# Performance work log

Hardware: AMD Instinct MI355X
Metric: run time of the kernel (lower is better)

The kernel has to match this reference:

```python
import jax, jax.numpy as jnp
import numpy as np

NEG_SLOPE = 0.2
EPS = 1e-16

N_NODES = 50000
N_EDGES = 1600000
IN_CH = 256
HID = 16
HEADS = 2


def setup_inputs() -> dict:
    key = jax.random.key(0)
    ks = jax.random.split(key, 12)
    s = lambda k, shape, scale=0.1: jax.random.normal(k, shape, dtype=jnp.float32) * scale
    x = jax.random.normal(ks[0], (N_NODES, IN_CH), dtype=jnp.float32)
    edge_index = jax.random.randint(ks[1], (2, N_EDGES), 0, N_NODES, dtype=jnp.int64)
    return {
        "x": x,
        "edge_index": edge_index,
        "W1": s(ks[2], (IN_CH, HEADS * HID)),
        "att_src1": s(ks[3], (HEADS, HID)),
        "att_dst1": s(ks[4], (HEADS, HID)),
        "b1": jnp.zeros((HEADS * HID,), jnp.float32),
        "W2": s(ks[5], (HEADS * HID, HID)),
        "att_src2": s(ks[6], (1, HID)),
        "att_dst2": s(ks[7], (1, HID)),
        "b2": jnp.zeros((HID,), jnp.float32),
        "Wm1": s(ks[8], (2 * HID, HID)),
        "bm1": jnp.zeros((HID,), jnp.float32),
        "Wm2": s(ks[9], (HID, 1)),
        "bm2": jnp.zeros((1,), jnp.float32),
    }


def gat_conv(x, src, dst, W, att_src, att_dst, bias, heads, out_ch, concat):
    # x: [N, F] -> h: [N, H, C]
    n = x.shape[0]
    h = (x @ W).reshape(n, heads, out_ch)
    # per-node attention logits [N, H]
    a_src = jnp.sum(h * att_src, axis=-1)
    a_dst = jnp.sum(h * att_dst, axis=-1)
    # per-edge logits: message j (src) -> i (dst); softmax grouped by dst
    e = a_src[src] + a_dst[dst]                      # [E, H]
    e = jax.nn.leaky_relu(e, NEG_SLOPE)
    e_max = jax.ops.segment_max(e, dst, num_segments=n)
    e_exp = jnp.exp(e - e_max[dst])
    denom = jax.ops.segment_sum(e_exp, dst, num_segments=n)
    alpha = e_exp / (denom[dst] + EPS)               # [E, H]
    msg = alpha[:, :, None] * h[src]                 # [E, H, C]
    out = jax.ops.segment_sum(msg, dst, num_segments=n)  # [N, H, C]
    out = out.reshape(n, heads * out_ch) if concat else out.mean(axis=1)
    return out + bias


def reference(x, edge_index, W1, att_src1, att_dst1, b1,
              W2, att_src2, att_dst2, b2, Wm1, bm1, Wm2, bm2):
    src, dst = edge_index[0], edge_index[1]
    # eval mode: feature/attention dropout are identity
    h = gat_conv(x, src, dst, W1, att_src1, att_dst1, b1, HEADS, HID, concat=True)
    h = jax.nn.elu(h)
    h = gat_conv(h, src, dst, W2, att_src2, att_dst2, b2, 1, HID, concat=False)
    # edge MLP on gathered (src, dst) node pairs
    ef = jnp.concatenate([h[src], h[dst]], axis=-1)  # [E, 2*HID]
    ef = jax.nn.relu(ef @ Wm1 + bm1)
    flow = (ef @ Wm2 + bm2).squeeze(-1)              # [E]
    return jax.nn.relu(flow)
```

## Files before the change

kernel.cpp:

```cpp
#include <hip/hip_runtime.h>
#include <hip/hip_bf16.h>
#include <hip/hip_fp16.h>

#define N_NODES 50000
#define N_EDGES 1600000
#define IN_CH 256
#define NEG_SLOPE 0.2f
#define EPS_F 1e-16f
#define CNT_PAD 16
#define CAP 128
#define NBK 196
#define CAPB 10240
#define PCHUNK 3125
#define KTILE 64
#define XS_PITCH (KTILE + 4)

__device__ __forceinline__ float lrelu(float x) {
    return x > 0.f ? x : NEG_SLOPE * x;
}

__device__ __forceinline__ float2 h2f(unsigned int w) {
    __half2 h;
    *reinterpret_cast<unsigned int*>(&h) = w;
    return __half22float2(h);
}

__device__ __forceinline__ unsigned int f2h2(float a, float b) {
    __half2 h = __floats2half2_rn(a, b);
    return *reinterpret_cast<unsigned int*>(&h);
}

__device__ __forceinline__ int detect_i64(const int* __restrict__ ei) {
    const int lane = threadIdx.x & 63;
    const unsigned long long b = __ballot(ei[2 * lane + 1] != 0);
    return b == 0ull ? 1 : 0;
}

__device__ __forceinline__ int ld_src(const int* ei, int f, int e) {
    return f ? ei[2 * (size_t)e] : ei[e];
}
__device__ __forceinline__ int ld_dst(const int* ei, int f, int e) {
    return f ? ei[2 * (size_t)N_EDGES + 2 * (size_t)e]
             : ei[(size_t)N_EDGES + e];
}

__global__ __launch_bounds__(1024) void k_part(const int* __restrict__ ei,
                                               int* __restrict__ gcnt,
                                               int2* __restrict__ bseg)
{
    __shared__ int hist[NBK];
    __shared__ int cur[NBK];
    const int t = threadIdx.x;
    const int f = detect_i64(ei);
    for (int j = t; j < NBK; j += 1024) hist[j] = 0;
    __syncthreads();
    const int e0 = blockIdx.x * PCHUNK;
    const int e1 = min(e0 + PCHUNK, N_EDGES);
    for (int e = e0 + t; e < e1; e += 1024)
        atomicAdd(&hist[ld_dst(ei, f, e) >> 8], 1);
    __syncthreads();
    for (int j = t; j < NBK; j += 1024)
        cur[j] = j * CAPB + atomicAdd(&gcnt[j], hist[j]);
    __syncthreads();
    for (int e = e0 + t; e < e1; e += 1024) {
        const int s = ld_src(ei, f, e);
        const int d = ld_dst(ei, f, e);
        const int bk = d >> 8;
        const int pos = atomicAdd(&cur[bk], 1);
        if (pos - bk * CAPB < CAPB) bseg[pos] = make_int2(s, d);
    }
}

__global__ __launch_bounds__(1024) void k_sub(const int* __restrict__ gcnt,
                                              const int2* __restrict__ bseg,
                                              int* __restrict__ cnt,
                                              int* __restrict__ csr_src)
{
    __shared__ int cur[256];
    const int b = blockIdx.x;
    const int t = threadIdx.x;
    if (t < 256) cur[t] = 0;
    __syncthreads();
    const int count = min(gcnt[b], CAPB);
    const int2* seg = bseg + (size_t)b * CAPB;
    for (int i = t; i < count; i += 1024) {
        const int2 e = seg[i];
        const int slot = atomicAdd(&cur[e.y & 255], 1);
        if (slot < CAP) csr_src[((size_t)e.y << 7) + slot] = e.x;
    }
    __syncthreads();
    if (t < 256) {
        const int n = b * 256 + t;
        if (n < N_NODES) cnt[(size_t)n * CNT_PAD] = min(cur[t], CAP);
    }
}

__global__ __launch_bounds__(256) void k1_gemm1(
    const float* __restrict__ x, const float* __restrict__ W1,
    const float* __restrict__ att_src1, const float* __restrict__ att_dst1,
    __half* __restrict__ h1, float* __restrict__ a_src1, float* __restrict__ a_dst1)
{
    __shared__ float w1s[IN_CH * 32];
    __shared__ float xs[64 * XS_PITCH];
    __shared__ float attss[32], attds[32];
    const int t = threadIdx.x;
    for (int i = t; i < IN_CH * 32; i += 256) w1s[i] = W1[i];
    if (t < 32) { attss[t] = att_src1[t]; attds[t] = att_dst1[t]; }
    const int row0 = blockIdx.x * 64;
    const int colq = t & 7, c4 = colq * 4;
    const int rp = t >> 3;
    const int r0 = rp * 2, r1 = r0 + 1;
    float4 a0 = make_float4(0.f, 0.f, 0.f, 0.f);
    float4 a1 = make_float4(0.f, 0.f, 0.f, 0.f);
    for (int kb = 0; kb < IN_CH; kb += KTILE) {
        __syncthreads();
        #pragma unroll
        for (int i = 0; i < 4; ++i) {
            const int idx = t + 256 * i;
            const int r = idx >> 4, p = idx & 15;
            const int row = row0 + r;
            float4 vv = make_float4(0.f, 0.f, 0.f, 0.f);
            if (row < N_NODES)
                vv = *(const float4*)(x + (size_t)row * IN_CH + kb + p * 4);
            *(float4*)(&xs[r * XS_PITCH + p * 4]) = vv;
        }
        __syncthreads();
        #pragma unroll 8
        for (int kt = 0; kt < KTILE; ++kt) {
            const float xv0 = xs[r0 * XS_PITCH + kt];
            const float xv1 = xs[r1 * XS_PITCH + kt];
            const float4 wv = *(const float4*)(&w1s[(kb + kt) * 32 + c4]);
            a0.x += xv0 * wv.x; a0.y += xv0 * wv.y;
            a0.z += xv0 * wv.z; a0.w += xv0 * wv.w;
            a1.x += xv1 * wv.x; a1.y += xv1 * wv.y;
            a1.z += xv1 * wv.z; a1.w += xv1 * wv.w;
        }
    }
    const int row_a = row0 + r0, row_b = row0 + r1;
    if (row_a < N_NODES) {
        uint2 p; p.x = f2h2(a0.x, a0.y); p.y = f2h2(a0.z, a0.w);
        *(uint2*)(h1 + (size_t)row_a * 32 + c4) = p;
    }
    if (row_b < N_NODES) {
        uint2 p; p.x = f2h2(a1.x, a1.y); p.y = f2h2(a1.z, a1.w);
        *(uint2*)(h1 + (size_t)row_b * 32 + c4) = p;
    }
    float sa0 = a0.x * attss[c4] + a0.y * attss[c4 + 1]
              + a0.z * attss[c4 + 2] + a0.w * attss[c4 + 3];
    float sd0 = a0.x * attds[c4] + a0.y * attds[c4 + 1]
              + a0.z * attds[c4 + 2] + a0.w * attds[c4 + 3];
    float sa1 = a1.x * attss[c4] + a1.y * attss[c4 + 1]
              + a1.z * attss[c4 + 2] + a1.w * attss[c4 + 3];
    float sd1 = a1.x * attds[c4] + a1.y * attds[c4 + 1]
              + a1.z * attds[c4 + 2] + a1.w * attds[c4 + 3];
    sa0 += __shfl_xor(sa0, 1); sa0 += __shfl_xor(sa0, 2);
    sd0 += __shfl_xor(sd0, 1); sd0 += __shfl_xor(sd0, 2);
    sa1 += __shfl_xor(sa1, 1); sa1 += __shfl_xor(sa1, 2);
    sd1 += __shfl_xor(sd1, 1); sd1 += __shfl_xor(sd1, 2);
    const int head = colq >> 2;
    if ((colq & 3) == 0) {
        if (row_a < N_NODES) {
            a_src1[row_a * 2 + head] = sa0;
            a_dst1[row_a * 2 + head] = sd0;
        }
        if (row_b < N_NODES) {
            a_src1[row_b * 2 + head] = sa1;
            a_dst1[row_b * 2 + head] = sd1;
        }
    }
}

__global__ __launch_bounds__(256) void k_agg1f(
    const int* __restrict__ cnt, const int* __restrict__ csr_src,
    const float* __restrict__ a_src1, const float* __restrict__ a_dst1,
    const __half* __restrict__ h1,
    const float* __restrict__ b1, const float* __restrict__ W2,
    const float* __restrict__ att_src2, const float* __restrict__ att_dst2,
    __half* __restrict__ h2, float* __restrict__ a_src2, float* __restrict__ a_dst2)
{
    __shared__ float w2s[32 * 16];
    __shared__ float b1s[32], as2[16], ad2[16];
    __shared__ float act_s[4][32];
    const int t = threadIdx.x;
    for (int i = t; i < 512; i += 256) w2s[i] = W2[i];
    if (t < 32) b1s[t] = b1[t];
    if (t < 16) { as2[t] = att_src2[t]; ad2[t] = att_dst2[t]; }

    const int wid = (blockIdx.x * 256 + t) >> 6;
    const int lane = t & 63;
    const int wv = t >> 6;
    const int active = (wid < N_NODES);
    const int len = active ? min(cnt[(size_t)wid * CNT_PAD], CAP) : 0;
    const int beg = wid << 7, end = beg + len;
    float2 ad = make_float2(0.f, 0.f);
    if (active) ad = *(const float2*)(a_dst1 + 2 * (size_t)wid);
    const int slot = lane >> 4, chp = lane & 15;
    const int head = chp >> 3;
    const float adh = head ? ad.y : ad.x;
    const int rep = ((chp & 7) == 0);
    const unsigned int* __restrict__ h1u = (const unsigned int*)h1;
    float accx = 0.f, accy = 0.f, sw = 0.f;
    int i = beg + slot;
    for (; i + 28 < end; i += 32) {
        int s[8]; float a[8]; unsigned int hw[8]; float w[8];
        #pragma unroll
        for (int j = 0; j < 8; ++j) s[j] = csr_src[i + 4 * j];
        #pragma unroll
        for (int j = 0; j < 8; ++j) a[j] = a_src1[2 * (size_t)s[j] + head];
        #pragma unroll
        for (int j = 0; j < 8; ++j) hw[j] = h1u[(size_t)s[j] * 16 + chp];
        #pragma unroll
        for (int j = 0; j < 8; ++j) w[j] = __expf(lrelu(a[j] + adh));
        float wsum = 0.f;
        #pragma unroll
        for (int j = 0; j < 8; ++j) {
            const float2 hf = h2f(hw[j]);
            wsum += w[j];
            accx += w[j] * hf.x; accy += w[j] * hf.y;
        }
        if (rep) sw += wsum;
    }
    for (; i + 12 < end; i += 16) {
        int s[4]; float a[4]; unsigned int hw[4]; float w[4];
        #pragma unroll
        for (int j = 0; j < 4; ++j) s[j] = csr_src[i + 4 * j];
        #pragma unroll
        for (int j = 0; j < 4; ++j) a[j] = a_src1[2 * (size_t)s[j] + head];
        #pragma unroll
        for (int j = 0; j < 4; ++j) hw[j] = h1u[(size_t)s[j] * 16 + chp];
        #pragma unroll
        for (int j = 0; j < 4; ++j) w[j] = __expf(lrelu(a[j] + adh));
        float wsum = 0.f;
        #pragma unroll
        for (int j = 0; j < 4; ++j) {
            const float2 hf = h2f(hw[j]);
            wsum += w[j];
            accx += w[j] * hf.x; accy += w[j] * hf.y;
        }
        if (rep) sw += wsum;
    }
    for (; i < end; i += 4) {
        const int s = csr_src[i];
        const float w = __expf(lrelu(a_src1[2 * (size_t)s + head] + adh));
        if (rep) sw += w;
        const float2 hf = h2f(h1u[(size_t)s * 16 + chp]);
        accx += w * hf.x; accy += w * hf.y;
    }
    sw += __shfl_xor(sw, 16); sw += __shfl_xor(sw, 32);
    const float swh = __shfl(sw, head << 3);
    accx += __shfl_xor(accx, 16); accx += __shfl_xor(accx, 32);
    accy += __shfl_xor(accy, 16); accy += __shfl_xor(accy, 32);
    const float inv = 1.f / (swh + EPS_F);
    if (lane < 16) {
        float ax = accx * inv + b1s[2 * chp];
        float ay = accy * inv + b1s[2 * chp + 1];
        ax = ax > 0.f ? ax : expm1f(ax);
        ay = ay > 0.f ? ay : expm1f(ay);
        act_s[wv][2 * chp] = ax;
        act_s[wv][2 * chp + 1] = ay;
    }
    __syncthreads();
    const int j = lane & 15;
    float acc2 = 0.f;
    #pragma unroll
    for (int k = 0; k < 32; ++k) acc2 += act_s[wv][k] * w2s[k * 16 + j];
    if (lane < 16 && active) h2[(size_t)wid * 16 + j] = __float2half(acc2);
    float sa = acc2 * as2[j], sd = acc2 * ad2[j];
    sa += __shfl_xor(sa, 1); sa += __shfl_xor(sa, 2);
    sa += __shfl_xor(sa, 4); sa += __shfl_xor(sa, 8);
    sd += __shfl_xor(sd, 1); sd += __shfl_xor(sd, 2);
    sd += __shfl_xor(sd, 4); sd += __shfl_xor(sd, 8);
    if (lane == 0 && active) { a_src2[wid] = sa; a_dst2[wid] = sd; }
}

__global__ __launch_bounds__(256) void k_agg2f(
    const int* __restrict__ cnt, const int* __restrict__ csr_src,
    const float* __restrict__ a_src2, const float* __restrict__ a_dst2,
    const __half* __restrict__ h2,
    const float* __restrict__ b2, const float* __restrict__ Wm1,
    const float* __restrict__ bm1,
    __half* __restrict__ u, __half* __restrict__ v)
{
    __shared__ float wa[16 * 16], wb[16 * 16];
    __shared__ float b2s[16], bm1s[16];
    __shared__ float act_s[4][16];
    const int t = threadIdx.x;
    if (t < 256) { wa[t] = Wm1[t]; wb[t] = Wm1[256 + t]; }
    if (t < 16) { b2s[t] = b2[t]; bm1s[t] = bm1[t]; }

    const int wid = (blockIdx.x * 256 + t) >> 6;
    const int lane = t & 63;
    const int wv = t >> 6;
    const int active = (wid < N_NODES);
    const int len = active ? min(cnt[(size_t)wid * CNT_PAD], CAP) : 0;
    const int beg = wid << 7, end = beg + len;
    const float ad = active ? a_dst2[wid] : 0.f;
    const int slot = lane >> 3, chp = lane & 7;
    const int rep = (chp == 0);
    const unsigned int* __restrict__ h2u = (const unsigned int*)h2;
    float accx = 0.f, accy = 0.f, sw = 0.f;
    int i = beg + slot;
    for (; i + 24 < end; i += 32) {
        int s[4]; float a[4]; unsigned int hw[4]; float w[4];
        #pragma unroll
        for (int j = 0; j < 4; ++j) s[j] = csr_src[i + 8 * j];
        #pragma unroll
        for (int j = 0; j < 4; ++j) a[j] = a_src2[s[j]];
        #pragma unroll
        for (int j = 0; j < 4; ++j) hw[j] = h2u[(size_t)s[j] * 8 + chp];
        #pragma unroll
        for (int j = 0; j < 4; ++j) w[j] = __expf(lrelu(a[j] + ad));
        float wsum = 0.f;
        #pragma unroll
        for (int j = 0; j < 4; ++j) {
            const float2 hf = h2f(hw[j]);
            wsum += w[j];
            accx += w[j] * hf.x; accy += w[j] * hf.y;
        }
        if (rep) sw += wsum;
    }
    for (; i < end; i += 8) {
        const int s = csr_src[i];
        const float w = __expf(lrelu(a_src2[s] + ad));
        if (rep) sw += w;
        const float2 hf = h2f(h2u[(size_t)s * 8 + chp]);
        accx += w * hf.x; accy += w * hf.y;
    }
    sw += __shfl_xor(sw, 8); sw += __shfl_xor(sw, 16); sw += __shfl_xor(sw, 32);
    const float swt = __shfl(sw, 0);
    accx += __shfl_xor(accx, 8); accx += __shfl_xor(accx, 16); accx += __shfl_xor(accx, 32);
    accy += __shfl_xor(accy, 8); accy += __shfl_xor(accy, 16); accy += __shfl_xor(accy, 32);
    const float inv = 1.f / (swt + EPS_F);
    if (lane < 8) {
        float2 o;
        o.x = accx * inv + b2s[2 * chp];
        o.y = accy * inv + b2s[2 * chp + 1];
        *(float2*)(&act_s[wv][2 * chp]) = o;
    }
    __syncthreads();
    const int c = lane & 15;
    float su = bm1s[c], sv = 0.f;
    #pragma unroll
    for (int k = 0; k < 16; ++k) {
        const float a = act_s[wv][k];
        su += a * wa[k * 16 + c];
        sv += a * wb[k * 16 + c];
    }
    if (lane < 16 && active) {
        u[(size_t)wid * 16 + c] = __float2half(su);
        v[(size_t)wid * 16 + c] = __float2half(sv);
    }
}

__global__ __launch_bounds__(256) void k7_lite(
    const int* __restrict__ ei,
    const __half* __restrict__ u, const __half* __restrict__ v,
    const float* __restrict__ Wm2, const float* __restrict__ bm2,
    float* __restrict__ out)
{
    __shared__ float wm2s[16];
    __shared__ float bm2s;
    const int t = threadIdx.x;
    const int f = detect_i64(ei);
    if (t < 16) wm2s[t] = Wm2[t];
    if (t == 0) bm2s = bm2[0];
    __syncthreads();
    const int e = blockIdx.x * 256 + t;
    if (e >= N_EDGES) return;
    const int s = ld_src(ei, f, e);
    const int d = ld_dst(ei, f, e);
    const uint4* up = (const uint4*)(u + (size_t)s * 16);
    const uint4* vp = (const uint4*)(v + (size_t)d * 16);
    const uint4 ua = up[0], ub = up[1];
    const uint4 va = vp[0], vb = vp[1];
    float fl = bm2s;
    unsigned int uw[8] = {ua.x, ua.y, ua.z, ua.w, ub.x, ub.y, ub.z, ub.w};
    unsigned int vw[8] = {va.x, va.y, va.z, va.w, vb.x, vb.y, vb.z, vb.w};
    #pragma unroll
    for (int i = 0; i < 8; ++i) {
        const float2 a = h2f(uw[i]);
        const float2 b = h2f(vw[i]);
        fl += fmaxf(a.x + b.x, 0.f) * wm2s[2 * i];
        fl += fmaxf(a.y + b.y, 0.f) * wm2s[2 * i + 1];
    }
    out[e] = fmaxf(fl, 0.f);
}

extern "C" void kernel_launch(void* const* d_in, const int* in_sizes, int n_in,
                              void* d_out, int out_size, void* d_ws, size_t ws_size,
                              hipStream_t stream)
{
    const float* x        = (const float*)d_in[0];
    const int*   ei       = (const int*)d_in[1];
    const float* W1       = (const float*)d_in[2];
    const float* att_src1 = (const float*)d_in[3];
    const float* att_dst1 = (const float*)d_in[4];
    const float* b1       = (const float*)d_in[5];
    const float* W2       = (const float*)d_in[6];
    const float* att_src2 = (const float*)d_in[7];
    const float* att_dst2 = (const float*)d_in[8];
    const float* b2       = (const float*)d_in[9];
    const float* Wm1      = (const float*)d_in[10];
    const float* bm1      = (const float*)d_in[11];
    const float* Wm2      = (const float*)d_in[12];
    const float* bm2      = (const float*)d_in[13];

    float* ws = (float*)d_ws;
    size_t off = 0;
    __half* h1 = (__half*)(ws + off); off += 16 * (size_t)N_NODES;
    float* a_src1 = ws + off; off += 2  * (size_t)N_NODES;
    float* a_dst1 = ws + off; off += 2  * (size_t)N_NODES;
    float* out1_dead = ws + off; off += 32 * (size_t)N_NODES;
    __half* h2 = (__half*)(ws + off); off += 16 * (size_t)N_NODES;
    float* a_src2 = ws + off; off += 1  * (size_t)N_NODES;
    float* a_dst2 = ws + off; off += 1  * (size_t)N_NODES;
    float* out2_dead = ws + off; off += 16 * (size_t)N_NODES;
    __half* u = (__half*)(ws + off); off += 8 * (size_t)N_NODES;
    __half* v = (__half*)(ws + off); off += 8 * (size_t)N_NODES;
    int* cnt     = (int*)(ws + off); off += (size_t)N_NODES * CNT_PAD;
    int* csr_src = (int*)(ws + off); off += (size_t)N_NODES * CAP;
    int* gcnt    = (int*)(ws + off); off += 256;
    int* flag    = (int*)(ws + off); off += 64;
    (void)out1_dead; (void)out2_dead; (void)flag;
    int2* bseg = (int2*)ws;

    hipMemsetAsync(gcnt, 0, 256 * sizeof(int), stream);
    k_part<<<(N_EDGES + PCHUNK - 1) / PCHUNK, 1024, 0, stream>>>(ei, gcnt, bseg);
    k_sub<<<NBK, 1024, 0, stream>>>(gcnt, bseg, cnt, csr_src);

    k1_gemm1<<<(N_NODES + 63) / 64, 256, 0, stream>>>(
        x, W1, att_src1, att_dst1, h1, a_src1, a_dst1);
    k_agg1f<<<(N_NODES + 3) / 4, 256, 0, stream>>>(
        cnt, csr_src, a_src1, a_dst1, h1, b1, W2, att_src2, att_dst2,
        h2, a_src2, a_dst2);
    k_agg2f<<<(N_NODES + 3) / 4, 256, 0, stream>>>(
        cnt, csr_src, a_src2, a_dst2, h2, b2, Wm1, bm1, u, v);
    k7_lite<<<(N_EDGES + 255) / 256, 256, 0, stream>>>(
        ei, u, v, Wm2, bm2, (float*)d_out);
}
```

Measured before the change: 259.3 us.

## Map one node per 16-lane group in layer-1 aggregation and cache edges in registers

The layer-1 aggregation kernel now gives each 16-lane group its own destination node, four nodes per wave and 16 per block, instead of one node per 64-lane wave. This removes the cross-slot shuffle reductions and the underused lanes on short adjacency lists, but lanes in a wave now diverge on list length and idle lanes are masked. The partition kernel loads each thread's edges once into registers and reuses them for both the histogram and scatter passes, removing a second global read of edge_index. The bucketed edge scratch also gets its own workspace region instead of aliasing the start of the workspace, and the dead buffers are dropped.

Result: faster. 251.6 us (-3.0%).

```diff
diff --git a/kernel.cpp b/kernel.cpp
--- a/kernel.cpp
+++ b/kernel.cpp
@@ -56,18 +56,26 @@
     __syncthreads();
     const int e0 = blockIdx.x * PCHUNK;
     const int e1 = min(e0 + PCHUNK, N_EDGES);
-    for (int e = e0 + t; e < e1; e += 1024)
-        atomicAdd(&hist[ld_dst(ei, f, e) >> 8], 1);
+    int es[4], ed[4];
+    int ne = 0;
+    #pragma unroll
+    for (int q = 0; q < 4; ++q) {
+        const int e = e0 + t + 1024 * q;
+        if (e < e1) {
+            es[ne] = ld_src(ei, f, e);
+            ed[ne] = ld_dst(ei, f, e);
+            ++ne;
+        }
+    }
+    for (int q = 0; q < ne; ++q) atomicAdd(&hist[ed[q] >> 8], 1);
     __syncthreads();
     for (int j = t; j < NBK; j += 1024)
         cur[j] = j * CAPB + atomicAdd(&gcnt[j], hist[j]);
     __syncthreads();
-    for (int e = e0 + t; e < e1; e += 1024) {
-        const int s = ld_src(ei, f, e);
-        const int d = ld_dst(ei, f, e);
-        const int bk = d >> 8;
+    for (int q = 0; q < ne; ++q) {
+        const int bk = ed[q] >> 8;
         const int pos = atomicAdd(&cur[bk], 1);
-        if (pos - bk * CAPB < CAPB) bseg[pos] = make_int2(s, d);
+        if (pos - bk * CAPB < CAPB) bseg[pos] = make_int2(es[q], ed[q]);
     }
 }
 
@@ -180,97 +188,69 @@
 {
     __shared__ float w2s[32 * 16];
     __shared__ float b1s[32], as2[16], ad2[16];
-    __shared__ float act_s[4][32];
+    __shared__ float act_s[16][33];
     const int t = threadIdx.x;
     for (int i = t; i < 512; i += 256) w2s[i] = W2[i];
     if (t < 32) b1s[t] = b1[t];
     if (t < 16) { as2[t] = att_src2[t]; ad2[t] = att_dst2[t]; }
 
-    const int wid = (blockIdx.x * 256 + t) >> 6;
     const int lane = t & 63;
     const int wv = t >> 6;
-    const int active = (wid < N_NODES);
-    const int len = active ? min(cnt[(size_t)wid * CNT_PAD], CAP) : 0;
-    const int beg = wid << 7, end = beg + len;
-    float2 ad = make_float2(0.f, 0.f);
-    if (active) ad = *(const float2*)(a_dst1 + 2 * (size_t)wid);
-    const int slot = lane >> 4, chp = lane & 15;
+    const int g = lane >> 4;
+    const int chp = lane & 15;
     const int head = chp >> 3;
-    const float adh = head ? ad.y : ad.x;
-    const int rep = ((chp & 7) == 0);
+    const int node = blockIdx.x * 16 + wv * 4 + g;
+    const int active = (node < N_NODES);
+    const int len = active ? min(cnt[(size_t)node * CNT_PAD], CAP) : 0;
+    const int beg = node << 7;
+    const float adh = active ? a_dst1[2 * (size_t)node + head] : 0.f;
     const unsigned int* __restrict__ h1u = (const unsigned int*)h1;
     float accx = 0.f, accy = 0.f, sw = 0.f;
-    int i = beg + slot;
-    for (; i + 28 < end; i += 32) {
+    for (int bi = 0; __any(bi < len); bi += 8) {
         int s[8]; float a[8]; unsigned int hw[8]; float w[8];
         #pragma unroll
-        for (int j = 0; j < 8; ++j) s[j] = csr_src[i + 4 * j];
+        for (int j = 0; j < 8; ++j) {
+            int sv = csr_src[beg + bi + j];
+            s[j] = (bi + j < len) ? sv : 0;
+        }
         #pragma unroll
         for (int j = 0; j < 8; ++j) a[j] = a_src1[2 * (size_t)s[j] + head];
         #pragma unroll
         for (int j = 0; j < 8; ++j) hw[j] = h1u[(size_t)s[j] * 16 + chp];
         #pragma unroll
-        for (int j = 0; j < 8; ++j) w[j] = __expf(lrelu(a[j] + adh));
-        float wsum = 0.f;
+        for (int j = 0; j < 8; ++j)
+            w[j] = (bi + j < len) ? __expf(lrelu(a[j] + adh)) : 0.f;
         #pragma unroll
         for (int j = 0; j < 8; ++j) {
             const float2 hf = h2f(hw[j]);
-            wsum += w[j];
+            sw += w[j];
             accx += w[j] * hf.x; accy += w[j] * hf.y;
         }
-        if (rep) sw += wsum;
-    }
-    for (; i + 12 < end; i += 16) {
-        int s[4]; float a[4]; unsigned int hw[4]; float w[4];
-        #pragma unroll
-        for (int j = 0; j < 4; ++j) s[j] = csr_src[i + 4 * j];
-        #pragma unroll
-        for (int j = 0; j < 4; ++j) a[j] = a_src1[2 * (size_t)s[j] + head];
-        #pragma unroll
-        for (int j = 0; j < 4; ++j) hw[j] = h1u[(size_t)s[j] * 16 + chp];
-        #pragma unroll
-        for (int j = 0; j < 4; ++j) w[j] = __expf(lrelu(a[j] + adh));
-        float wsum = 0.f;
-        #pragma unroll
-        for (int j = 0; j < 4; ++j) {
-            const float2 hf = h2f(hw[j]);
-            wsum += w[j];
-            accx += w[j] * hf.x; accy += w[j] * hf.y;
-        }
-        if (rep) sw += wsum;
-    }
-    for (; i < end; i += 4) {
-        const int s = csr_src[i];
-        const float w = __expf(lrelu(a_src1[2 * (size_t)s + head] + adh));
-        if (rep) sw += w;
-        const float2 hf = h2f(h1u[(size_t)s * 16 + chp]);
-        accx += w * hf.x; accy += w * hf.y;
-    }
-    sw += __shfl_xor(sw, 16); sw += __shfl_xor(sw, 32);
-    const float swh = __shfl(sw, head << 3);
-    accx += __shfl_xor(accx, 16); accx += __shfl_xor(accx, 32);
-    accy += __shfl_xor(accy, 16); accy += __shfl_xor(accy, 32);
-    const float inv = 1.f / (swh + EPS_F);
-    if (lane < 16) {
+    }
+    const float inv = 1.f / (sw + EPS_F);
+    const int nl = wv * 4 + g;
+    {
         float ax = accx * inv + b1s[2 * chp];
         float ay = accy * inv + b1s[2 * chp + 1];
         ax = ax > 0.f ? ax : expm1f(ax);
         ay = ay > 0.f ? ay : expm1f(ay);
-        act_s[wv][2 * chp] = ax;
-        act_s[wv][2 * chp + 1] = ay;
-    }
-    __syncthreads();
-    const int j = lane & 15;
+        act_s[nl][2 * chp] = ax;
+        act_s[nl][2 * chp + 1] = ay;
+    }
+    __syncthreads();
+    const int nn = t >> 4;
+    const int j2 = t & 15;
+    const int node2 = blockIdx.x * 16 + nn;
     float acc2 = 0.f;
     #pragma unroll
-    for (int k = 0; k < 32; ++k) acc2 += act_s[wv][k] * w2s[k * 16 + j];
-    if (lane < 16 && active) h2[(size_t)wid * 16 + j] = __float2half(acc2);
-    float sa = acc2 * as2[j], sd = acc2 * ad2[j];
+    for (int k = 0; k < 32; ++k) acc2 += act_s[nn][k] * w2s[k * 16 + j2];
+    if (node2 < N_NODES) h2[(size_t)node2 * 16 + j2] = __float2half(acc2);
+    float sa = acc2 * as2[j2], sd = acc2 * ad2[j2];
     sa += __shfl_xor(sa, 1); sa += __shfl_xor(sa, 2);
     sa += __shfl_xor(sa, 4); sa += __shfl_xor(sa, 8);
     sd += __shfl_xor(sd, 1); sd += __shfl_xor(sd, 2);
     sd += __shfl_xor(sd, 4); sd += __shfl_xor(sd, 8);
-    if (lane == 0 && active) { a_src2[wid] = sa; a_dst2[wid] = sd; }
+    if (j2 == 0 && node2 < N_NODES) { a_src2[node2] = sa; a_dst2[node2] = sd; }
 }
 
 __global__ __launch_bounds__(256) void k_agg2f(
@@ -410,19 +390,15 @@
     __half* h1 = (__half*)(ws + off); off += 16 * (size_t)N_NODES;
     float* a_src1 = ws + off; off += 2  * (size_t)N_NODES;
     float* a_dst1 = ws + off; off += 2  * (size_t)N_NODES;
-    float* out1_dead = ws + off; off += 32 * (size_t)N_NODES;
-    __half* h2 = (__half*)(ws + off); off += 16 * (size_t)N_NODES;
+    __half* h2 = (__half*)(ws + off); off += 8 * (size_t)N_NODES;
     float* a_src2 = ws + off; off += 1  * (size_t)N_NODES;
     float* a_dst2 = ws + off; off += 1  * (size_t)N_NODES;
-    float* out2_dead = ws + off; off += 16 * (size_t)N_NODES;
     __half* u = (__half*)(ws + off); off += 8 * (size_t)N_NODES;
     __half* v = (__half*)(ws + off); off += 8 * (size_t)N_NODES;
-    int* cnt     = (int*)(ws + off); off += (size_t)N_NODES * CNT_PAD;
-    int* csr_src = (int*)(ws + off); off += (size_t)N_NODES * CAP;
-    int* gcnt    = (int*)(ws + off); off += 256;
-    int* flag    = (int*)(ws + off); off += 64;
-    (void)out1_dead; (void)out2_dead; (void)flag;
-    int2* bseg = (int2*)ws;
+    int* cnt     = (int*)(ws + off);  off += (size_t)N_NODES * CNT_PAD;
+    int* csr_src = (int*)(ws + off);  off += (size_t)N_NODES * CAP;
+    int2* bseg   = (int2*)(ws + off); off += (size_t)NBK * CAPB * 2;
+    int* gcnt    = (int*)(ws + off);  off += 256;
 
     hipMemsetAsync(gcnt, 0, 256 * sizeof(int), stream);
     k_part<<<(N_EDGES + PCHUNK - 1) / PCHUNK, 1024, 0, stream>>>(ei, gcnt, bseg);
@@ -430,7 +406,7 @@
 
     k1_gemm1<<<(N_NODES + 63) / 64, 256, 0, stream>>>(
         x, W1, att_src1, att_dst1, h1, a_src1, a_dst1);
-    k_agg1f<<<(N_NODES + 3) / 4, 256, 0, stream>>>(
+    k_agg1f<<<(N_NODES + 15) / 16, 256, 0, stream>>>(
         cnt, csr_src, a_src1, a_dst1, h1, b1, W2, att_src2, att_dst2,
         h2, a_src2, a_dst2);
     k_agg2f<<<(N_NODES + 3) / 4, 256, 0, stream>>>(
```
